# Optimization experiments

Hardware: AMD Instinct MI355X
Metric: run time of the kernel (lower is better)

Reference implementation:

```python
import jax, jax.numpy as jnp
import numpy as np

B, T, K = 8192, 256, 16
N_TRANS = 4  # 0: s2u, 1: u2s_n0, 2: u2s_n1_d2, 3: u2s_n1_dgt2  (DistanceCRF)


def setup_inputs() -> dict:
    key = jax.random.key(0)
    ks = jax.random.split(key, 8)
    emissions = jax.random.normal(ks[0], (B, T, K), dtype=jnp.float32)
    tags = jax.random.randint(ks[1], (B, T), 0, K, dtype=jnp.int32)
    who2who = jax.random.randint(ks[2], (B, T - 1), 0, 2, dtype=jnp.int32)
    init_count = jax.random.randint(ks[3], (B, T - 1), 0, 2, dtype=jnp.int32)
    distance = jax.random.randint(ks[4], (B, T - 1), 0, 2, dtype=jnp.int32)
    class_weights = jax.random.uniform(ks[5], (K,), dtype=jnp.float32, minval=0.5, maxval=2.0)
    trans_stack = jax.random.normal(ks[6], (N_TRANS, K, K), dtype=jnp.float32) * 0.1
    start_scores = jax.random.normal(ks[7], (K,), dtype=jnp.float32) * 0.1
    return {
        'emissions': emissions, 'tags': tags, 'who2who': who2who,
        'init_count': init_count, 'distance': distance,
        'class_weights': class_weights, 'trans_stack': trans_stack,
        'start_scores': start_scores,
    }


def _trans_index(who2who, init_count, distance):
    # Mirrors MultiTurnCRF._get_trans for variant='DistanceCRF':
    #   w==1 -> s2u; w==0 & init_count==0 -> u2s_n0;
    #   w==0 & init>0 & distance==0 -> u2s_n1_d2; else u2s_n1_dgt2
    return jnp.where(who2who == 1, 0,
           jnp.where(init_count == 0, 1,
           jnp.where(distance == 0, 2, 3)))


def _crf_seq(em, tags, tidx, class_weights, trans_stack, start_scores):
    # em: [T, K], tags: [T], tidx: [T-1]
    w = class_weights[tags]                               # [T]
    em_gold = jnp.take_along_axis(em, tags[:, None], axis=1)[:, 0]   # [T]
    tr_gold = trans_stack[tidx, tags[:-1], tags[1:]]      # [T-1]
    gold = w[0] * (start_scores[tags[0]] + em_gold[0]) \
           + jnp.sum(w[1:] * (tr_gold + em_gold[1:]))

    def step(alpha, xs):
        ti, e = xs
        tr = trans_stack[ti]                              # [K, K]
        alpha = jax.nn.logsumexp(alpha[:, None] + tr + e[None, :], axis=0)
        return alpha, None

    alpha0 = start_scores + em[0]
    alphaT, _ = jax.lax.scan(step, alpha0, (tidx, em[1:]))
    log_Z = jax.nn.logsumexp(alphaT)
    return gold, log_Z


def reference(emissions, tags, who2who, init_count, distance,
              class_weights, trans_stack, start_scores):
    tidx = _trans_index(who2who, init_count, distance)    # [B, T-1]
    gold, log_Z = jax.vmap(_crf_seq, in_axes=(0, 0, 0, None, None, None))(
        emissions, tags, tidx, class_weights, trans_stack, start_scores)
    return gold, log_Z
```

## Files before the change

### kernel.cpp

```cpp
#include <hip/hip_runtime.h>

#define T_LEN 256
#define K 16
#define B_TOT 8192
#define RSCALE 3.2734375f

__global__ __launch_bounds__(256) void pack_ctrl(
    const int* __restrict__ tags, const int* __restrict__ w2w,
    const int* __restrict__ ic,   const int* __restrict__ ds,
    const float* __restrict__ cw, const float* __restrict__ trans,
    unsigned char* __restrict__ ctrl, float* __restrict__ goldt)
{
    int idx = blockIdx.x * 256 + threadIdx.x;
    int b = idx >> 8, t = idx & 255;
    int tag = tags[idx];
    unsigned char byte = (unsigned char)tag;
    float g = 0.0f;
    if (t > 0) {
        int off = b * (T_LEN - 1) + (t - 1);
        int tidx = (w2w[off] == 1) ? 0 : ((ic[off] == 0) ? 1 : ((ds[off] == 0) ? 2 : 3));
        byte |= (unsigned char)(tidx << 4);
        int tp = tags[idx - 1];
        g = cw[tag] * trans[tidx * 256 + tp * 16 + tag];
    }
    ctrl[idx]  = byte;
    goldt[idx] = g;
}

__device__ __forceinline__ float ror1(float x) {
    int xi = __float_as_int(x);
    int r = __builtin_amdgcn_update_dpp(xi, xi, 0x121, 0xF, 0xF, false);
    return __int_as_float(r);
}
__device__ __forceinline__ float ror8(float x) {
    int xi = __float_as_int(x);
    int r = __builtin_amdgcn_update_dpp(xi, xi, 0x128, 0xF, 0xF, false);
    return __int_as_float(r);
}

__global__ __launch_bounds__(256, 2) void crf_fwd(
    const float* __restrict__ emissions,
    const float* __restrict__ class_weights,
    const float* __restrict__ trans_stack,
    const float* __restrict__ start_scores,
    const uint4* __restrict__ ctrl16,
    const float4* __restrict__ goldt4,
    float*       __restrict__ out)
{
    __shared__ float trans_lds[4 * K * K];
    for (int idx = threadIdx.x; idx < 4 * K * K; idx += blockDim.x)
        trans_lds[idx] = trans_stack[idx];
    __syncthreads();

    const int j   = threadIdx.x & 15;
    const int seq = (blockIdx.x * blockDim.x + threadIdx.x) >> 4;

    int pr    = __builtin_amdgcn_update_dpp(j, j, 0x121, 0xF, 0xF, false);
    int delta = (pr - j) & 15;

    float D[4][16];
#pragma unroll
    for (int c = 0; c < 4; ++c)
#pragma unroll
        for (int r = 0; r < 16; ++r)
            D[c][r] = __expf(trans_lds[c * 256 + ((j + r * delta) & 15) * 16 + j]);

    const float cw_j    = class_weights[j];
    const float start_j = start_scores[j];
    const float* em_ptr = emissions + seq * (T_LEN * K) + j;

    float u = 0.0f, gold = 0.0f, logC = 0.0f;

    float emb[16];
#pragma unroll
    for (int k = 0; k < 16; ++k) emb[k] = em_ptr[k * K];
    uint4 pkt = ctrl16[seq * 16 + 0];
    float gtf[16];
    {
        float4 q0 = goldt4[seq * 64 + 0], q1 = goldt4[seq * 64 + 1];
        float4 q2 = goldt4[seq * 64 + 2], q3 = goldt4[seq * 64 + 3];
        gtf[0]=q0.x; gtf[1]=q0.y; gtf[2]=q0.z; gtf[3]=q0.w;
        gtf[4]=q1.x; gtf[5]=q1.y; gtf[6]=q1.z; gtf[7]=q1.w;
        gtf[8]=q2.x; gtf[9]=q2.y; gtf[10]=q2.z; gtf[11]=q2.w;
        gtf[12]=q3.x; gtf[13]=q3.y; gtf[14]=q3.z; gtf[15]=q3.w;
    }

    for (int blk = 0; blk < 16; ++blk) {
        int nb = (blk < 15) ? blk + 1 : 15;
        float embn[16];
#pragma unroll
        for (int k = 0; k < 16; ++k) embn[k] = em_ptr[(nb * 16 + k) * K];
        uint4 pktn = ctrl16[seq * 16 + nb];
        float4 q0 = goldt4[seq * 64 + nb * 4 + 0], q1 = goldt4[seq * 64 + nb * 4 + 1];
        float4 q2 = goldt4[seq * 64 + nb * 4 + 2], q3 = goldt4[seq * 64 + nb * 4 + 3];

#pragma unroll
        for (int k = 0; k < 16; ++k) {
            unsigned w = (k < 4) ? pkt.x : (k < 8) ? pkt.y : (k < 12) ? pkt.z : pkt.w;
            unsigned byte = (w >> (8 * (k & 3))) & 0xFFu;
            int tag  = (int)(byte & 15u);
            int tidx = (int)(byte >> 4);

            if (blk == 0 && k == 0) {
                u    = __expf(start_j + emb[0]);
                gold = (j == tag) ? cw_j * (start_j + emb[0]) : 0.0f;
            } else {
                bool tlo = tidx < 2, is0 = tidx == 0, is2 = tidx == 2;
                float s0 = 0.0f, s1 = 0.0f;
                float ua = u, ub = ror8(u);
#pragma unroll
                for (int r = 0; r < 8; ++r) {
                    if (r) { ua = ror1(ua); ub = ror1(ub); }
                    float e0a = is0 ? D[0][r] : D[1][r];
                    float e0b = is2 ? D[2][r] : D[3][r];
                    float e0  = tlo ? e0a : e0b;
                    float e1a = is0 ? D[0][r + 8] : D[1][r + 8];
                    float e1b = is2 ? D[2][r + 8] : D[3][r + 8];
                    float e1  = tlo ? e1a : e1b;
                    s0 = fmaf(ua, e0, s0);
                    s1 = fmaf(ub, e1, s1);
                }
                u = (s0 + s1) * __expf(emb[k] - RSCALE);
                if (j == tag) gold += gtf[k] + cw_j * emb[k];
            }
        }

        {
            float mx = u;
#pragma unroll
            for (int m = 1; m < 16; m <<= 1)
                mx = fmaxf(mx, __shfl_xor(mx, m, 64));
            int ex;
            (void)frexpf(mx, &ex);
            u = ldexpf(u, -ex);
            logC += (float)ex * 0.693147180559945f;
        }

#pragma unroll
        for (int k = 0; k < 16; ++k) emb[k] = embn[k];
        pkt = pktn;
        gtf[0]=q0.x; gtf[1]=q0.y; gtf[2]=q0.z; gtf[3]=q0.w;
        gtf[4]=q1.x; gtf[5]=q1.y; gtf[6]=q1.z; gtf[7]=q1.w;
        gtf[8]=q2.x; gtf[9]=q2.y; gtf[10]=q2.z; gtf[11]=q2.w;
        gtf[12]=q3.x; gtf[13]=q3.y; gtf[14]=q3.z; gtf[15]=q3.w;
    }

    float su = u, sg = gold;
#pragma unroll
    for (int m = 1; m < 16; m <<= 1) {
        su += __shfl_xor(su, m, 64);
        sg += __shfl_xor(sg, m, 64);
    }

    if (j == 0) {
        out[seq]         = sg;
        out[B_TOT + seq] = logf(su) + 255.0f * RSCALE + logC;
    }
}

extern "C" void kernel_launch(void* const* d_in, const int* in_sizes, int n_in,
                              void* d_out, int out_size, void* d_ws, size_t ws_size,
                              hipStream_t stream) {
    const float* emissions     = (const float*)d_in[0];
    const int*   tags          = (const int*)  d_in[1];
    const int*   who2who       = (const int*)  d_in[2];
    const int*   init_count    = (const int*)  d_in[3];
    const int*   distance      = (const int*)  d_in[4];
    const float* class_weights = (const float*)d_in[5];
    const float* trans_stack   = (const float*)d_in[6];
    const float* start_scores  = (const float*)d_in[7];
    float* out = (float*)d_out;

    unsigned char* ctrl  = (unsigned char*)d_ws;
    float*         goldt = (float*)((char*)d_ws + B_TOT * T_LEN);

    hipLaunchKernelGGL(pack_ctrl, dim3(B_TOT), dim3(256), 0, stream,
                       tags, who2who, init_count, distance,
                       class_weights, trans_stack, ctrl, goldt);

    hipLaunchKernelGGL(crf_fwd, dim3(B_TOT * 16 / 256), dim3(256), 0, stream,
                       emissions, class_weights, trans_stack, start_scores,
                       (const uint4*)ctrl, (const float4*)goldt, out);
}
```

Before: 273.2 us.

## Use packed fp16 dot2 recurrence and split gold-score reduction into a separate kernel

```diff
diff --git a/kernel.cpp b/kernel.cpp
--- a/kernel.cpp
+++ b/kernel.cpp
@@ -1,161 +1,164 @@
 #include <hip/hip_runtime.h>
 
 #define T_LEN 256
-#define K 16
 #define B_TOT 8192
 #define RSCALE 3.2734375f
+#define L2E    1.44269504f
+#define LN2    0.693147180559945f
+
+typedef __attribute__((ext_vector_type(2))) _Float16 h2;
+
+__device__ __forceinline__ h2 pkrtz(float lo, float hi) {
+    return __builtin_bit_cast(h2, __builtin_amdgcn_cvt_pkrtz(lo, hi));
+}
+__device__ __forceinline__ float ror8f(float x) {
+    int xi = __float_as_int(x);
+    int r = __builtin_amdgcn_update_dpp(xi, xi, 0x128, 0xF, 0xF, false);
+    return __int_as_float(r);
+}
+__device__ __forceinline__ h2 ror1h(h2 x) {
+    int xi = __builtin_bit_cast(int, x);
+    int r = __builtin_amdgcn_update_dpp(xi, xi, 0x121, 0xF, 0xF, false);
+    return __builtin_bit_cast(h2, r);
+}
 
 __global__ __launch_bounds__(256) void pack_ctrl(
     const int* __restrict__ tags, const int* __restrict__ w2w,
     const int* __restrict__ ic,   const int* __restrict__ ds,
     const float* __restrict__ cw, const float* __restrict__ trans,
-    unsigned char* __restrict__ ctrl, float* __restrict__ goldt)
+    const float* __restrict__ start,
+    unsigned char* __restrict__ ctrl, float* __restrict__ goldp)
 {
     int idx = blockIdx.x * 256 + threadIdx.x;
     int b = idx >> 8, t = idx & 255;
     int tag = tags[idx];
     unsigned char byte = (unsigned char)tag;
-    float g = 0.0f;
-    if (t > 0) {
+    float g;
+    if (t == 0) {
+        g = cw[tag] * start[tag];
+    } else {
         int off = b * (T_LEN - 1) + (t - 1);
         int tidx = (w2w[off] == 1) ? 0 : ((ic[off] == 0) ? 1 : ((ds[off] == 0) ? 2 : 3));
         byte |= (unsigned char)(tidx << 4);
-        int tp = tags[idx - 1];
-        g = cw[tag] * trans[tidx * 256 + tp * 16 + tag];
+        g = cw[tag] * trans[tidx * 256 + tags[idx - 1] * 16 + tag];
     }
     ctrl[idx]  = byte;
-    goldt[idx] = g;
+    goldp[idx] = g;
 }
 
-__device__ __forceinline__ float ror1(float x) {
-    int xi = __float_as_int(x);
-    int r = __builtin_amdgcn_update_dpp(xi, xi, 0x121, 0xF, 0xF, false);
-    return __int_as_float(r);
-}
-__device__ __forceinline__ float ror8(float x) {
-    int xi = __float_as_int(x);
-    int r = __builtin_amdgcn_update_dpp(xi, xi, 0x128, 0xF, 0xF, false);
-    return __int_as_float(r);
-}
-
-__global__ __launch_bounds__(256, 2) void crf_fwd(
-    const float* __restrict__ emissions,
-    const float* __restrict__ class_weights,
-    const float* __restrict__ trans_stack,
-    const float* __restrict__ start_scores,
-    const uint4* __restrict__ ctrl16,
-    const float4* __restrict__ goldt4,
-    float*       __restrict__ out)
+__global__ __launch_bounds__(256, 2) void crf_rec(
+    const float* __restrict__ em, const float* __restrict__ trans,
+    const float* __restrict__ start, const float* __restrict__ cw,
+    const unsigned char* __restrict__ ctrl,
+    float* __restrict__ gev, float* __restrict__ out)
 {
-    __shared__ float trans_lds[4 * K * K];
-    for (int idx = threadIdx.x; idx < 4 * K * K; idx += blockDim.x)
-        trans_lds[idx] = trans_stack[idx];
+    __shared__ float tl[1024];
+    for (int i = threadIdx.x; i < 1024; i += 256) tl[i] = trans[i];
     __syncthreads();
 
     const int j   = threadIdx.x & 15;
-    const int seq = (blockIdx.x * blockDim.x + threadIdx.x) >> 4;
+    const int seq = (blockIdx.x * 256 + threadIdx.x) >> 4;
 
     int pr    = __builtin_amdgcn_update_dpp(j, j, 0x121, 0xF, 0xF, false);
     int delta = (pr - j) & 15;
 
-    float D[4][16];
+    h2 D[4][8];
 #pragma unroll
     for (int c = 0; c < 4; ++c)
 #pragma unroll
-        for (int r = 0; r < 16; ++r)
-            D[c][r] = __expf(trans_lds[c * 256 + ((j + r * delta) & 15) * 16 + j]);
+        for (int r = 0; r < 8; ++r) {
+            float lo = __expf(tl[c * 256 + ((j + r * delta) & 15) * 16 + j]);
+            float hi = __expf(tl[c * 256 + ((j + (r + 8) * delta) & 15) * 16 + j]);
+            D[c][r] = pkrtz(lo, hi);
+        }
 
-    const float cw_j    = class_weights[j];
-    const float start_j = start_scores[j];
-    const float* em_ptr = emissions + seq * (T_LEN * K) + j;
+    const float cw_j = cw[j];
+    const float st_j = start[j];
+    const float* ep  = em + (size_t)seq * 4096 + j;
+    const uint4* cp  = (const uint4*)(ctrl + (size_t)seq * 256);
 
-    float u = 0.0f, gold = 0.0f, logC = 0.0f;
+    float emr[16];
+#pragma unroll
+    for (int k = 0; k < 16; ++k) emr[k] = ep[k * 16];
+    uint4 cq = cp[0], cqn = cp[1];
 
-    float emb[16];
-#pragma unroll
-    for (int k = 0; k < 16; ++k) emb[k] = em_ptr[k * K];
-    uint4 pkt = ctrl16[seq * 16 + 0];
-    float gtf[16];
+    float u, ge, logC = 5.545177444479562f;
     {
-        float4 q0 = goldt4[seq * 64 + 0], q1 = goldt4[seq * 64 + 1];
-        float4 q2 = goldt4[seq * 64 + 2], q3 = goldt4[seq * 64 + 3];
-        gtf[0]=q0.x; gtf[1]=q0.y; gtf[2]=q0.z; gtf[3]=q0.w;
-        gtf[4]=q1.x; gtf[5]=q1.y; gtf[6]=q1.z; gtf[7]=q1.w;
-        gtf[8]=q2.x; gtf[9]=q2.y; gtf[10]=q2.z; gtf[11]=q2.w;
-        gtf[12]=q3.x; gtf[13]=q3.y; gtf[14]=q3.z; gtf[15]=q3.w;
+        int tag0 = (int)(cq.x & 15u);
+        u  = __expf(st_j + emr[0]) * 0.00390625f;
+        ge = (j == tag0) ? cw_j * emr[0] : 0.0f;
+        emr[0] = ep[16 * 16];
     }
 
-    for (int blk = 0; blk < 16; ++blk) {
-        int nb = (blk < 15) ? blk + 1 : 15;
-        float embn[16];
+    auto STEP = [&](int t, int k, bool pf) __attribute__((always_inline)) {
+        unsigned dw = (k < 4) ? cq.x : (k < 8) ? cq.y : (k < 12) ? cq.z : cq.w;
+        int sh = 8 * (k & 3);
+        int tag   = (int)((dw >> sh) & 15u);
+        bool modd = ((dw >> (sh + 4)) & 1u) != 0u;
+        bool mhi  = ((dw >> (sh + 5)) & 1u) != 0u;
+
+        float uh = ror8f(u);
+        h2 P = pkrtz(u, uh);
+        float s = 0.0f;
 #pragma unroll
-        for (int k = 0; k < 16; ++k) embn[k] = em_ptr[(nb * 16 + k) * K];
-        uint4 pktn = ctrl16[seq * 16 + nb];
-        float4 q0 = goldt4[seq * 64 + nb * 4 + 0], q1 = goldt4[seq * 64 + nb * 4 + 1];
-        float4 q2 = goldt4[seq * 64 + nb * 4 + 2], q3 = goldt4[seq * 64 + nb * 4 + 3];
+        for (int r = 0; r < 8; ++r) {
+            if (r) P = ror1h(P);
+            h2 e01 = modd ? D[1][r] : D[0][r];
+            h2 e23 = modd ? D[3][r] : D[2][r];
+            h2 e   = mhi ? e23 : e01;
+            s = __builtin_amdgcn_fdot2(P, e, s, false);
+        }
+        float exf = __builtin_exp2f(fmaf(emr[k], L2E, -RSCALE * L2E));
+        if (j == tag) ge = fmaf(cw_j, emr[k], ge);
+        u = s * exf;
+        if (pf) emr[k] = ep[(size_t)(t + 16) * 16];
+        if ((k & 7) == 7) {
+            float mx = u;
+            mx = fmaxf(mx, __shfl_xor(mx, 1, 64));
+            mx = fmaxf(mx, __shfl_xor(mx, 2, 64));
+            mx = fmaxf(mx, __shfl_xor(mx, 4, 64));
+            mx = fmaxf(mx, __shfl_xor(mx, 8, 64));
+            int e2; (void)frexpf(mx, &e2);
+            u = ldexpf(u, -e2 - 4);
+            logC += (float)(e2 + 4) * LN2;
+        }
+    };
 
 #pragma unroll
-        for (int k = 0; k < 16; ++k) {
-            unsigned w = (k < 4) ? pkt.x : (k < 8) ? pkt.y : (k < 12) ? pkt.z : pkt.w;
-            unsigned byte = (w >> (8 * (k & 3))) & 0xFFu;
-            int tag  = (int)(byte & 15u);
-            int tidx = (int)(byte >> 4);
+    for (int k = 1; k < 16; ++k) STEP(k, k, true);
+    for (int blk = 1; blk < 15; ++blk) {
+        cq = cqn;
+        cqn = cp[blk + 1];
+#pragma unroll
+        for (int k = 0; k < 16; ++k) STEP(blk * 16 + k, k, true);
+    }
+    cq = cqn;
+#pragma unroll
+    for (int k = 0; k < 16; ++k) STEP(240 + k, k, false);
 
-            if (blk == 0 && k == 0) {
-                u    = __expf(start_j + emb[0]);
-                gold = (j == tag) ? cw_j * (start_j + emb[0]) : 0.0f;
-            } else {
-                bool tlo = tidx < 2, is0 = tidx == 0, is2 = tidx == 2;
-                float s0 = 0.0f, s1 = 0.0f;
-                float ua = u, ub = ror8(u);
-#pragma unroll
-                for (int r = 0; r < 8; ++r) {
-                    if (r) { ua = ror1(ua); ub = ror1(ub); }
-                    float e0a = is0 ? D[0][r] : D[1][r];
-                    float e0b = is2 ? D[2][r] : D[3][r];
-                    float e0  = tlo ? e0a : e0b;
-                    float e1a = is0 ? D[0][r + 8] : D[1][r + 8];
-                    float e1b = is2 ? D[2][r + 8] : D[3][r + 8];
-                    float e1  = tlo ? e1a : e1b;
-                    s0 = fmaf(ua, e0, s0);
-                    s1 = fmaf(ub, e1, s1);
-                }
-                u = (s0 + s1) * __expf(emb[k] - RSCALE);
-                if (j == tag) gold += gtf[k] + cw_j * emb[k];
-            }
-        }
-
-        {
-            float mx = u;
-#pragma unroll
-            for (int m = 1; m < 16; m <<= 1)
-                mx = fmaxf(mx, __shfl_xor(mx, m, 64));
-            int ex;
-            (void)frexpf(mx, &ex);
-            u = ldexpf(u, -ex);
-            logC += (float)ex * 0.693147180559945f;
-        }
-
-#pragma unroll
-        for (int k = 0; k < 16; ++k) emb[k] = embn[k];
-        pkt = pktn;
-        gtf[0]=q0.x; gtf[1]=q0.y; gtf[2]=q0.z; gtf[3]=q0.w;
-        gtf[4]=q1.x; gtf[5]=q1.y; gtf[6]=q1.z; gtf[7]=q1.w;
-        gtf[8]=q2.x; gtf[9]=q2.y; gtf[10]=q2.z; gtf[11]=q2.w;
-        gtf[12]=q3.x; gtf[13]=q3.y; gtf[14]=q3.z; gtf[15]=q3.w;
-    }
-
-    float su = u, sg = gold;
+    float su = u, gs = ge;
 #pragma unroll
     for (int m = 1; m < 16; m <<= 1) {
         su += __shfl_xor(su, m, 64);
-        sg += __shfl_xor(sg, m, 64);
+        gs += __shfl_xor(gs, m, 64);
     }
-
     if (j == 0) {
-        out[seq]         = sg;
+        gev[seq] = gs;
         out[B_TOT + seq] = logf(su) + 255.0f * RSCALE + logC;
     }
+}
+
+__global__ __launch_bounds__(256) void gold_red(
+    const float* __restrict__ goldp, const float* __restrict__ gev,
+    float* __restrict__ out)
+{
+    int b = blockIdx.x * 4 + (threadIdx.x >> 6);
+    int l = threadIdx.x & 63;
+    const float* p = goldp + (size_t)b * 256;
+    float s = (p[l] + p[l + 64]) + (p[l + 128] + p[l + 192]);
+#pragma unroll
+    for (int m = 1; m < 64; m <<= 1) s += __shfl_xor(s, m, 64);
+    if (l == 0) out[b] = s + gev[b];
 }
 
 extern "C" void kernel_launch(void* const* d_in, const int* in_sizes, int n_in,
@@ -171,14 +174,19 @@
     const float* start_scores  = (const float*)d_in[7];
     float* out = (float*)d_out;
 
-    unsigned char* ctrl  = (unsigned char*)d_ws;
-    float*         goldt = (float*)((char*)d_ws + B_TOT * T_LEN);
+    char* ws = (char*)d_ws;
+    unsigned char* ctrl  = (unsigned char*)ws;
+    float* goldp = (float*)(ws + (2 << 20));
+    float* gev   = (float*)(ws + (10 << 20));
 
     hipLaunchKernelGGL(pack_ctrl, dim3(B_TOT), dim3(256), 0, stream,
                        tags, who2who, init_count, distance,
-                       class_weights, trans_stack, ctrl, goldt);
+                       class_weights, trans_stack, start_scores, ctrl, goldp);
 
-    hipLaunchKernelGGL(crf_fwd, dim3(B_TOT * 16 / 256), dim3(256), 0, stream,
-                       emissions, class_weights, trans_stack, start_scores,
-                       (const uint4*)ctrl, (const float4*)goldt, out);
+    hipLaunchKernelGGL(crf_rec, dim3(B_TOT * 16 / 256), dim3(256), 0, stream,
+                       emissions, trans_stack, start_scores, class_weights,
+                       ctrl, gev, out);
+
+    hipLaunchKernelGGL(gold_red, dim3(B_TOT / 4), dim3(256), 0, stream,
+                       goldp, gev, out);
 }
```

Result: faster. 250.9 us (-8.2%).
